# Kernel tuning notes

Hardware: AMD Instinct MI355X
Metric: run time of the kernel (lower is better)

## Reference

```python
import jax, jax.numpy as jnp
import numpy as np

E = 1024      # embedding_size
K = 64        # key_size
D = 64        # head_size
S = 1024      # context_size
V = 32000     # vocab_size
H = 16        # layer_size (heads per layer)
L = 8         # num_layers
B = 2


def _pe():
    pos = jnp.arange(S, dtype=jnp.float32)[:, None]
    i = jnp.arange(E, dtype=jnp.float32)[None, :]
    ang = pos / jnp.power(10000.0, 2.0 * i / E)
    return jnp.where((jnp.arange(E) % 2 == 0)[None, :], jnp.sin(ang), jnp.cos(ang))


def setup_inputs() -> dict:
    key = jax.random.key(0)
    ks = iter(jax.random.split(key, 32))
    s = 0.02
    n = lambda shape: jax.random.normal(next(ks), shape, dtype=jnp.float32) * s
    inp = {
        "tokens": jax.random.randint(next(ks), (B, S), 0, V),
        "emb": n((V, E)),
        "pe": _pe(),
        "k1w": n((L, H, K, E)), "k1b": n((L, H, K)),
        "k2w": n((L, H, K, K)), "k2b": n((L, H, K)),
        "q1w": n((L, H, K, E)), "q1b": n((L, H, K)),
        "q2w": n((L, H, K, K)), "q2b": n((L, H, K)),
        "vw": n((L, H, D, E)), "vb": n((L, H, D)),
        "lnw": jnp.ones((L, E), jnp.float32), "lnb": jnp.zeros((L, E), jnp.float32),
        "p1w": n((L, E, E)), "p1b": n((L, E)),
        "p2w": n((L, E, E)), "p2b": n((L, E)),
        "predw": n((V, E)), "predb": n((V,)),
    }
    return inp


def reference(tokens, emb, pe, k1w, k1b, k2w, k2b, q1w, q1b, q2w, q2b,
              vw, vb, lnw, lnb, p1w, p1b, p2w, p2b, predw, predb):
    relu = jax.nn.relu
    x = emb[tokens] + pe[:tokens.shape[1]]                       # [B,S,E]
    seq = tokens.shape[1]
    # Faithful to original: tril (past+diag) gets the -1e10 penalty.
    mask = jnp.tril(jnp.ones((seq, seq), x.dtype)) * -1e10
    for l in range(L):
        # two-layer ReLU MLPs for K and Q, batched over heads
        k = relu(jnp.einsum('bse,hke->bhsk', x, k1w[l]) + k1b[l][None, :, None, :])
        k = relu(jnp.einsum('bhsk,hjk->bhsj', k, k2w[l]) + k2b[l][None, :, None, :])
        q = relu(jnp.einsum('bse,hke->bhsk', x, q1w[l]) + q1b[l][None, :, None, :])
        q = relu(jnp.einsum('bhsk,hjk->bhsj', q, q2w[l]) + q2b[l][None, :, None, :])
        v = jnp.einsum('bse,hde->bhsd', x, vw[l]) + vb[l][None, :, None, :]
        scores = jnp.einsum('bhsk,bhtk->bhst', q, k) / (K ** 0.5) + mask
        w = jax.nn.softmax(scores, axis=-1)
        o = jnp.einsum('bhst,bhtd->bhsd', w, v)                  # [B,H,S,D]
        o = o.transpose(0, 2, 1, 3).reshape(x.shape[0], seq, H * D)
        y = x + o
        mu = y.mean(-1, keepdims=True)
        var = ((y - mu) ** 2).mean(-1, keepdims=True)
        yn = (y - mu) / jnp.sqrt(var + 1e-5) * lnw[l] + lnb[l]
        h1 = relu(yn @ p1w[l].T + p1b[l])
        x = relu(h1 @ p2w[l].T + p2b[l])
    logits = x @ predw.T + predb                                 # [B,S,V]
    return logits
```

## Files before the change

### kernel.cpp

```cpp
#include <hip/hip_runtime.h>


typedef __attribute__((ext_vector_type(8))) short bf16x8;
typedef __attribute__((ext_vector_type(4))) float f32x4;

#define L_ 8
#define S_ 1024
#define E_ 1024
#define B_ 2
#define H_ 16
#define V_ 32000
#define M_ 2048

__device__ __forceinline__ unsigned short f2b(float f) {
  union { float f; unsigned int u; } v; v.f = f;
  unsigned int r = v.u + 0x7FFFu + ((v.u >> 16) & 1u);
  return (unsigned short)(r >> 16);
}

#define GLDS16(gptr, lptr)                                                            \
  __builtin_amdgcn_global_load_lds(                                                   \
      (const __attribute__((address_space(1))) unsigned int*)(gptr),                  \
      (__attribute__((address_space(3))) unsigned int*)(lptr), 16, 0, 0)

__global__ void cvt_kernel(const float* __restrict__ src, unsigned short* __restrict__ dst) {
  size_t i = ((size_t)blockIdx.x * 256 + threadIdx.x) * 4;
  float4 v = *(const float4*)(src + i);
  unsigned short* d = dst + i;
  d[0] = f2b(v.x); d[1] = f2b(v.y); d[2] = f2b(v.z); d[3] = f2b(v.w);
}

__global__ void cvt_seg_kernel(const float* __restrict__ src, unsigned short* __restrict__ dst,
                               int perLayer, int dstStride, int dstOff) {
  size_t i = ((size_t)blockIdx.x * 256 + threadIdx.x) * 4;
  int l = (int)(i / perLayer);
  int off = (int)(i - (size_t)l * perLayer);
  float4 v = *(const float4*)(src + i);
  unsigned short* d = dst + (size_t)l * dstStride + dstOff + off;
  d[0] = f2b(v.x); d[1] = f2b(v.y); d[2] = f2b(v.z); d[3] = f2b(v.w);
}

__global__ void biascat_kernel(const float* __restrict__ k1b, const float* __restrict__ q1b,
                               const float* __restrict__ vb, float* __restrict__ bcat) {
  int i = blockIdx.x * 256 + threadIdx.x;
  int l = i / 3072, j = i - l * 3072;
  float v;
  if (j < 1024)      v = k1b[l * 1024 + j];
  else if (j < 2048) v = q1b[l * 1024 + j - 1024];
  else               v = vb [l * 1024 + j - 2048];
  bcat[i] = v;
}

__global__ void embed_kernel(const int* __restrict__ tokens, const float* __restrict__ emb,
                             const float* __restrict__ pe, float* __restrict__ x32,
                             unsigned short* __restrict__ xb) {
  int row = blockIdx.x;
  int s = row & (S_ - 1);
  int e0 = threadIdx.x * 4;
  int tok = tokens[row];
  float4 ev = *(const float4*)(emb + (size_t)tok * E_ + e0);
  float4 pv = *(const float4*)(pe + (size_t)s * E_ + e0);
  float4 v; v.x = ev.x + pv.x; v.y = ev.y + pv.y; v.z = ev.z + pv.z; v.w = ev.w + pv.w;
  *(float4*)(x32 + (size_t)row * E_ + e0) = v;
  ushort4 o; o.x = f2b(v.x); o.y = f2b(v.y); o.z = f2b(v.z); o.w = f2b(v.w);
  *(ushort4*)(xb + (size_t)row * E_ + e0) = o;
}

template <int BM, int RELU, int OBF, int OF32>
__global__ __launch_bounds__(256) void gemm97(
    const unsigned short* __restrict__ A, const unsigned short* __restrict__ W,
    const float* __restrict__ bias, unsigned short* __restrict__ Cb,
    float* __restrict__ Cf, int K, int N, int reluN) {
  constexpr int AR = BM / 64;
  constexpr int FM = (BM == 128) ? 4 : 2;
  constexpr int WMS = (BM == 128) ? 64 : 32;
  __shared__ __align__(16) unsigned short sA[BM * 32];
  __shared__ __align__(16) unsigned short sB[128 * 32];
  const int tid = threadIdx.x;
  const int lane = tid & 63, wave = tid >> 6;
  const int l16 = lane & 15, lhi = lane >> 4;

  const int gx = gridDim.x, nwg = gx * gridDim.y;
  int o = blockIdx.y * gx + blockIdx.x;
  int wg = ((nwg & 7) == 0) ? ((o & 7) * (nwg >> 3) + (o >> 3)) : o;
  const int row0 = (wg % gx) * BM, col0 = (wg / gx) * 128;

  const int wm = (wave >> 1) * WMS, wn = (wave & 1) * 64;

  const int srow = wave * 16 + (lane >> 2);
  const int scol = (lane & 3) * 8;

  f32x4 acc[FM][4] = {};

  for (int k0 = 0; k0 < K; k0 += 32) {
#pragma unroll
    for (int r = 0; r < AR; r++)
      GLDS16(A + (size_t)(row0 + r * 64 + srow) * K + k0 + scol,
             sA + r * 2048 + wave * 512);
#pragma unroll
    for (int r = 0; r < 2; r++)
      GLDS16(W + (size_t)(col0 + r * 64 + srow) * K + k0 + scol,
             sB + r * 2048 + wave * 512);
    __syncthreads();

    bf16x8 af[FM], bf[4];
#pragma unroll
    for (int i = 0; i < FM; i++)
      af[i] = *(const bf16x8*)(sA + (wm + i * 16 + l16) * 32 + lhi * 8);
#pragma unroll
    for (int j = 0; j < 4; j++)
      bf[j] = *(const bf16x8*)(sB + (wn + j * 16 + l16) * 32 + lhi * 8);
#pragma unroll
    for (int i = 0; i < FM; i++)
#pragma unroll
      for (int j = 0; j < 4; j++)
        acc[i][j] = __builtin_amdgcn_mfma_f32_16x16x32_bf16(bf[j], af[i], acc[i][j], 0, 0, 0);
    __syncthreads();
  }

#pragma unroll
  for (int j = 0; j < 4; j++) {
    const int colb = col0 + wn + j * 16 + lhi * 4;
    const float4 bv = *(const float4*)(bias + colb);
    const bool dorelu = (RELU == 1) || (RELU == 2 && colb < reluN);
#pragma unroll
    for (int i = 0; i < FM; i++) {
      const int row = row0 + wm + i * 16 + l16;
      float v0 = acc[i][j][0] + bv.x, v1 = acc[i][j][1] + bv.y;
      float v2 = acc[i][j][2] + bv.z, v3 = acc[i][j][3] + bv.w;
      if (dorelu) {
        v0 = fmaxf(v0, 0.f); v1 = fmaxf(v1, 0.f);
        v2 = fmaxf(v2, 0.f); v3 = fmaxf(v3, 0.f);
      }
      if (OBF) {
        ushort4 ob; ob.x = f2b(v0); ob.y = f2b(v1); ob.z = f2b(v2); ob.w = f2b(v3);
        *(ushort4*)(Cb + (size_t)row * N + colb) = ob;
      }
      if (OF32) {
        float4 of; of.x = v0; of.y = v1; of.z = v2; of.w = v3;
        *(float4*)(Cf + (size_t)row * N + colb) = of;
      }
    }
  }
}

__global__ __launch_bounds__(256) void k2q2_kernel(
    const unsigned short* __restrict__ kqv, const unsigned short* __restrict__ wk2,
    const unsigned short* __restrict__ wq2, const float* __restrict__ k2b,
    const float* __restrict__ q2b, unsigned short* __restrict__ kbuf,
    unsigned short* __restrict__ qbuf) {
  const int m0 = blockIdx.x * 64;
  const int h = blockIdx.y;
  const int which = blockIdx.z;
  const unsigned short* Ap = kqv + (which ? 1024 : 0) + h * 64;
  const unsigned short* Wp = (which ? wq2 : wk2) + h * 4096;
  const float* bias = (which ? q2b : k2b) + h * 64;
  unsigned short* out = (which ? qbuf : kbuf) + h * 64;
  const int lane = threadIdx.x & 63, wave = threadIdx.x >> 6;
  const int l16 = lane & 15, lhi = lane >> 4;
  const int mw = m0 + wave * 16;

  f32x4 acc[4] = {};
#pragma unroll
  for (int ks = 0; ks < 2; ks++) {
    bf16x8 a = *(const bf16x8*)(Ap + (size_t)(mw + l16) * 3072 + ks * 32 + (lhi << 3));
#pragma unroll
    for (int j = 0; j < 4; j++) {
      bf16x8 b = *(const bf16x8*)(Wp + (j * 16 + l16) * 64 + ks * 32 + (lhi << 3));
      acc[j] = __builtin_amdgcn_mfma_f32_16x16x32_bf16(a, b, acc[j], 0, 0, 0);
    }
  }
#pragma unroll
  for (int j = 0; j < 4; j++) {
    float bv = bias[j * 16 + l16];
#pragma unroll
    for (int r = 0; r < 4; r++) {
      int row = mw + (lhi << 2) + r;
      float v = fmaxf(acc[j][r] + bv, 0.f);
      out[(size_t)row * 1024 + j * 16 + l16] = f2b(v);
    }
  }
}

__global__ __launch_bounds__(256) void attn_kernel(
    const unsigned short* __restrict__ qbuf,
    const unsigned short* __restrict__ kbuf,
    const unsigned short* __restrict__ kqv,
    float* __restrict__ o32) {
  constexpr int LD = 72;
  __shared__ __align__(16) unsigned short sK[64 * LD];
  __shared__ __align__(16) unsigned short sV[64 * LD];
  __shared__ __align__(16) unsigned short sP[4 * 16 * LD];
  const int bx = blockIdx.x, h = blockIdx.y, b = blockIdx.z;
  const int tid = threadIdx.x, lane = tid & 63, wave = tid >> 6;
  const int l16 = lane & 15, lhi = lane >> 4;
  const int base = b * S_;

  const int qrow = bx * 64 + wave * 16 + l16;
  bf16x8 aq[2];
#pragma unroll
  for (int ks = 0; ks < 2; ks++)
    aq[ks] = *(const bf16x8*)(qbuf + (size_t)(base + qrow) * 1024 + h * 64 + ks * 32 + (lhi << 3));

  f32x4 oacc[4] = {};
  float mrun[4], lrun[4];
#pragma unroll
  for (int r = 0; r < 4; r++) { mrun[r] = -1e10f; lrun[r] = 0.f; }
  const int srow_base = bx * 64 + wave * 16 + (lhi << 2);

  for (int t0 = 0; t0 < S_; t0 += 64) {
    uint4 rk[2], rv[2];
#pragma unroll
    for (int r = 0; r < 2; r++) {
      int c = r * 256 + tid;
      int trow = c >> 3, c8 = (c & 7) << 3;
      rk[r] = *(const uint4*)(kbuf + (size_t)(base + t0 + trow) * 1024 + h * 64 + c8);
      rv[r] = *(const uint4*)(kqv + (size_t)(base + t0 + trow) * 3072 + 2048 + h * 64 + c8);
    }
    __syncthreads();
#pragma unroll
    for (int r = 0; r < 2; r++) {
      int c = r * 256 + tid;
      int trow = c >> 3, c8 = (c & 7) << 3;
      *(uint4*)(sK + trow * LD + c8) = rk[r];
      const unsigned short* ts = (const unsigned short*)&rv[r];
#pragma unroll
      for (int j = 0; j < 8; j++) sV[(c8 + j) * LD + trow] = ts[j];
    }
    __syncthreads();

    f32x4 sacc[4] = {};
#pragma unroll
    for (int ks = 0; ks < 2; ks++) {
#pragma unroll
      for (int nt = 0; nt < 4; nt++) {
        bf16x8 bk = *(const bf16x8*)(sK + (nt * 16 + l16) * LD + ks * 32 + (lhi << 3));
        sacc[nt] = __builtin_amdgcn_mfma_f32_16x16x32_bf16(aq[ks], bk, sacc[nt], 0, 0, 0);
      }
    }
    float p[4][4];
#pragma unroll
    for (int nt = 0; nt < 4; nt++) {
      int tcol = t0 + nt * 16 + l16;
#pragma unroll
      for (int r = 0; r < 4; r++) {
        float v = sacc[nt][r] * 0.125f;
        if (tcol <= srow_base + r) v = -1e10f;
        p[nt][r] = v;
      }
    }
#pragma unroll
    for (int r = 0; r < 4; r++) {
      float m = fmaxf(fmaxf(p[0][r], p[1][r]), fmaxf(p[2][r], p[3][r]));
#pragma unroll
      for (int off = 1; off < 16; off <<= 1) m = fmaxf(m, __shfl_xor(m, off, 16));
      float mnew = fmaxf(mrun[r], m);
      float alpha = __expf(mrun[r] - mnew);
      mrun[r] = mnew;
      float rs = 0.f;
#pragma unroll
      for (int nt = 0; nt < 4; nt++) {
        float e = __expf(p[nt][r] - mnew);
        p[nt][r] = e; rs += e;
      }
#pragma unroll
      for (int off = 1; off < 16; off <<= 1) rs += __shfl_xor(rs, off, 16);
      lrun[r] = lrun[r] * alpha + rs;
      oacc[0][r] *= alpha; oacc[1][r] *= alpha; oacc[2][r] *= alpha; oacc[3][r] *= alpha;
    }
    unsigned short* sPw = sP + wave * 16 * LD;
#pragma unroll
    for (int nt = 0; nt < 4; nt++)
#pragma unroll
      for (int r = 0; r < 4; r++)
        sPw[((lhi << 2) + r) * LD + nt * 16 + l16] = f2b(p[nt][r]);
#pragma unroll
    for (int ks = 0; ks < 2; ks++) {
      bf16x8 ap = *(const bf16x8*)(sPw + l16 * LD + ks * 32 + (lhi << 3));
#pragma unroll
      for (int nt = 0; nt < 4; nt++) {
        bf16x8 bv = *(const bf16x8*)(sV + (nt * 16 + l16) * LD + ks * 32 + (lhi << 3));
        oacc[nt] = __builtin_amdgcn_mfma_f32_16x16x32_bf16(ap, bv, oacc[nt], 0, 0, 0);
      }
    }
  }
#pragma unroll
  for (int nt = 0; nt < 4; nt++) {
#pragma unroll
    for (int r = 0; r < 4; r++) {
      int row = srow_base + r;
      o32[(size_t)(base + row) * 1024 + h * 64 + nt * 16 + l16] = oacc[nt][r] / lrun[r];
    }
  }
}

__global__ __launch_bounds__(256) void ln_kernel(
    const float* __restrict__ x32, const float* __restrict__ o32,
    const float* __restrict__ lnw, const float* __restrict__ lnb,
    unsigned short* __restrict__ yn) {
  __shared__ float red[8];
  const int row = blockIdx.x, tid = threadIdx.x;
  const int lane = tid & 63, wave = tid >> 6;
  const int e0 = tid * 4;
  float4 xv = *(const float4*)(x32 + (size_t)row * E_ + e0);
  float4 ov = *(const float4*)(o32 + (size_t)row * E_ + e0);
  float y0 = xv.x + ov.x, y1 = xv.y + ov.y, y2 = xv.z + ov.z, y3 = xv.w + ov.w;
  float s = y0 + y1 + y2 + y3;
  float sq = y0 * y0 + y1 * y1 + y2 * y2 + y3 * y3;
#pragma unroll
  for (int off = 32; off > 0; off >>= 1) {
    s += __shfl_xor(s, off, 64);
    sq += __shfl_xor(sq, off, 64);
  }
  if (lane == 0) { red[wave * 2] = s; red[wave * 2 + 1] = sq; }
  __syncthreads();
  float ts = red[0] + red[2] + red[4] + red[6];
  float tsq = red[1] + red[3] + red[5] + red[7];
  float mu = ts * (1.f / E_);
  float var = tsq * (1.f / E_) - mu * mu;
  float rstd = rsqrtf(var + 1e-5f);
  float4 gv = *(const float4*)(lnw + e0);
  float4 bv = *(const float4*)(lnb + e0);
  ushort4 o;
  o.x = f2b((y0 - mu) * rstd * gv.x + bv.x);
  o.y = f2b((y1 - mu) * rstd * gv.y + bv.y);
  o.z = f2b((y2 - mu) * rstd * gv.z + bv.z);
  o.w = f2b((y3 - mu) * rstd * gv.w + bv.w);
  *(ushort4*)(yn + (size_t)row * E_ + e0) = o;
}

extern "C" void kernel_launch(void* const* d_in, const int* in_sizes, int n_in,
                              void* d_out, int out_size, void* d_ws, size_t ws_size,
                              hipStream_t stream) {
  const int* tokens  = (const int*)d_in[0];
  const float* emb   = (const float*)d_in[1];
  const float* pe    = (const float*)d_in[2];
  const float* k1w   = (const float*)d_in[3];
  const float* k1b   = (const float*)d_in[4];
  const float* k2w   = (const float*)d_in[5];
  const float* k2b   = (const float*)d_in[6];
  const float* q1w   = (const float*)d_in[7];
  const float* q1b   = (const float*)d_in[8];
  const float* q2w   = (const float*)d_in[9];
  const float* q2b   = (const float*)d_in[10];
  const float* vw    = (const float*)d_in[11];
  const float* vb    = (const float*)d_in[12];
  const float* lnw   = (const float*)d_in[13];
  const float* lnb   = (const float*)d_in[14];
  const float* p1w   = (const float*)d_in[15];
  const float* p1b   = (const float*)d_in[16];
  const float* p2w   = (const float*)d_in[17];
  const float* p2b   = (const float*)d_in[18];
  const float* predw = (const float*)d_in[19];
  const float* predb = (const float*)d_in[20];
  float* out = (float*)d_out;

  char* p = (char*)d_ws;
  auto alloc = [&](size_t bytes) -> char* {
    char* r = p; p += (bytes + 255) & ~(size_t)255; return r;
  };
  unsigned short* wcat  = (unsigned short*)alloc((size_t)L_ * 3072 * 1024 * 2);
  unsigned short* wk2   = (unsigned short*)alloc((size_t)L_ * H_ * 64 * 64 * 2);
  unsigned short* wq2   = (unsigned short*)alloc((size_t)L_ * H_ * 64 * 64 * 2);
  unsigned short* wp1   = (unsigned short*)alloc((size_t)L_ * 1024 * 1024 * 2);
  unsigned short* wp2   = (unsigned short*)alloc((size_t)L_ * 1024 * 1024 * 2);
  unsigned short* wpred = (unsigned short*)alloc((size_t)V_ * 1024 * 2);
  float*          bcat  = (float*)alloc((size_t)L_ * 3072 * 4);
  float*          x32   = (float*)alloc((size_t)M_ * 1024 * 4);
  unsigned short* xb    = (unsigned short*)alloc((size_t)M_ * 1024 * 2);
  unsigned short* kqv   = (unsigned short*)alloc((size_t)M_ * 3072 * 2);
  unsigned short* kbuf  = (unsigned short*)alloc((size_t)M_ * 1024 * 2);
  unsigned short* qbuf  = (unsigned short*)alloc((size_t)M_ * 1024 * 2);
  float*          o32   = (float*)alloc((size_t)M_ * 1024 * 4);
  unsigned short* yn    = (unsigned short*)alloc((size_t)M_ * 1024 * 2);
  unsigned short* h1    = (unsigned short*)alloc((size_t)M_ * 1024 * 2);
  if ((size_t)(p - (char*)d_ws) > ws_size) return;

  cvt_seg_kernel<<<8192, 256, 0, stream>>>(k1w, wcat, 1048576, 3145728, 0);
  cvt_seg_kernel<<<8192, 256, 0, stream>>>(q1w, wcat, 1048576, 3145728, 1048576);
  cvt_seg_kernel<<<8192, 256, 0, stream>>>(vw,  wcat, 1048576, 3145728, 2097152);
  cvt_kernel<<<512, 256, 0, stream>>>(k2w, wk2);
  cvt_kernel<<<512, 256, 0, stream>>>(q2w, wq2);
  cvt_kernel<<<8192, 256, 0, stream>>>(p1w, wp1);
  cvt_kernel<<<8192, 256, 0, stream>>>(p2w, wp2);
  cvt_kernel<<<32000, 256, 0, stream>>>(predw, wpred);
  biascat_kernel<<<96, 256, 0, stream>>>(k1b, q1b, vb, bcat);

  embed_kernel<<<M_, 256, 0, stream>>>(tokens, emb, pe, x32, xb);

  for (int l = 0; l < L_; l++) {
    const unsigned short* wcat_l = wcat + (size_t)l * 3072 * 1024;
    const float* bcat_l = bcat + (size_t)l * 3072;
    const unsigned short* wk2_l = wk2 + (size_t)l * H_ * 64 * 64;
    const unsigned short* wq2_l = wq2 + (size_t)l * H_ * 64 * 64;
    const unsigned short* wp1_l = wp1 + (size_t)l * 1024 * 1024;
    const unsigned short* wp2_l = wp2 + (size_t)l * 1024 * 1024;

    gemm97<128, 2, 1, 0><<<dim3(16, 24), 256, 0, stream>>>(
        xb, wcat_l, bcat_l, kqv, nullptr, 1024, 3072, 2048);
    k2q2_kernel<<<dim3(32, 16, 2), 256, 0, stream>>>(
        kqv, wk2_l, wq2_l, k2b + l * 1024, q2b + l * 1024, kbuf, qbuf);
    attn_kernel<<<dim3(16, 16, 2), 256, 0, stream>>>(qbuf, kbuf, kqv, o32);
    ln_kernel<<<M_, 256, 0, stream>>>(x32, o32, lnw + l * 1024, lnb + l * 1024, yn);
    gemm97<64, 1, 1, 0><<<dim3(32, 8), 256, 0, stream>>>(
        yn, wp1_l, p1b + l * 1024, h1, nullptr, 1024, 1024, 0);
    gemm97<64, 1, 1, 1><<<dim3(32, 8), 256, 0, stream>>>(
        h1, wp2_l, p2b + l * 1024, xb, x32, 1024, 1024, 0);
  }

  gemm97<128, 0, 0, 1><<<dim3(16, 250), 256, 0, stream>>>(
      xb, wpred, predb, nullptr, out, 1024, V_, 0);
}
```

Measured before the change: 1.554 ms.

## Write transposed V from QKV GEMM and restructure attention to read global directly

The QKV GEMM epilogue now also writes V transposed per (batch, head) into a new buffer. The attention kernel drops its shared-memory staging of K and V and reads K and V^T fragments straight from global memory. It runs 128-thread blocks over 32-row query tiles, with a start offset that skips KV tiles the mask fully covers. The projection GEMMs switch to 64x64 tiles so more workgroups launch; the cost is scattered 2-byte stores for V^T and more global-load traffic in attention.

```diff
diff --git a/kernel.cpp b/kernel.cpp
--- a/kernel.cpp
+++ b/kernel.cpp
@@ -66,16 +66,18 @@
   *(ushort4*)(xb + (size_t)row * E_ + e0) = o;
 }
 
-template <int BM, int RELU, int OBF, int OF32>
+template <int BM, int BN, int RELU, int OBF, int OF32, int VT>
 __global__ __launch_bounds__(256) void gemm97(
     const unsigned short* __restrict__ A, const unsigned short* __restrict__ W,
     const float* __restrict__ bias, unsigned short* __restrict__ Cb,
-    float* __restrict__ Cf, int K, int N, int reluN) {
+    float* __restrict__ Cf, unsigned short* __restrict__ vTp,
+    int K, int N, int reluN) {
   constexpr int AR = BM / 64;
-  constexpr int FM = (BM == 128) ? 4 : 2;
-  constexpr int WMS = (BM == 128) ? 64 : 32;
+  constexpr int BR = BN / 64;
+  constexpr int FM = BM / 32;
+  constexpr int FN = BN / 32;
   __shared__ __align__(16) unsigned short sA[BM * 32];
-  __shared__ __align__(16) unsigned short sB[128 * 32];
+  __shared__ __align__(16) unsigned short sB[BN * 32];
   const int tid = threadIdx.x;
   const int lane = tid & 63, wave = tid >> 6;
   const int l16 = lane & 15, lhi = lane >> 4;
@@ -83,14 +85,14 @@
   const int gx = gridDim.x, nwg = gx * gridDim.y;
   int o = blockIdx.y * gx + blockIdx.x;
   int wg = ((nwg & 7) == 0) ? ((o & 7) * (nwg >> 3) + (o >> 3)) : o;
-  const int row0 = (wg % gx) * BM, col0 = (wg / gx) * 128;
-
-  const int wm = (wave >> 1) * WMS, wn = (wave & 1) * 64;
+  const int row0 = (wg % gx) * BM, col0 = (wg / gx) * BN;
+
+  const int wm = (wave >> 1) * (BM / 2), wn = (wave & 1) * (BN / 2);
 
   const int srow = wave * 16 + (lane >> 2);
   const int scol = (lane & 3) * 8;
 
-  f32x4 acc[FM][4] = {};
+  f32x4 acc[FM][FN] = {};
 
   for (int k0 = 0; k0 < K; k0 += 32) {
 #pragma unroll
@@ -98,28 +100,28 @@
       GLDS16(A + (size_t)(row0 + r * 64 + srow) * K + k0 + scol,
              sA + r * 2048 + wave * 512);
 #pragma unroll
-    for (int r = 0; r < 2; r++)
+    for (int r = 0; r < BR; r++)
       GLDS16(W + (size_t)(col0 + r * 64 + srow) * K + k0 + scol,
              sB + r * 2048 + wave * 512);
     __syncthreads();
 
-    bf16x8 af[FM], bf[4];
+    bf16x8 af[FM], bf[FN];
 #pragma unroll
     for (int i = 0; i < FM; i++)
       af[i] = *(const bf16x8*)(sA + (wm + i * 16 + l16) * 32 + lhi * 8);
 #pragma unroll
-    for (int j = 0; j < 4; j++)
+    for (int j = 0; j < FN; j++)
       bf[j] = *(const bf16x8*)(sB + (wn + j * 16 + l16) * 32 + lhi * 8);
 #pragma unroll
     for (int i = 0; i < FM; i++)
 #pragma unroll
-      for (int j = 0; j < 4; j++)
+      for (int j = 0; j < FN; j++)
         acc[i][j] = __builtin_amdgcn_mfma_f32_16x16x32_bf16(bf[j], af[i], acc[i][j], 0, 0, 0);
     __syncthreads();
   }
 
 #pragma unroll
-  for (int j = 0; j < 4; j++) {
+  for (int j = 0; j < FN; j++) {
     const int colb = col0 + wn + j * 16 + lhi * 4;
     const float4 bv = *(const float4*)(bias + colb);
     const bool dorelu = (RELU == 1) || (RELU == 2 && colb < reluN);
@@ -139,6 +141,14 @@
       if (OF32) {
         float4 of; of.x = v0; of.y = v1; of.z = v2; of.w = v3;
         *(float4*)(Cf + (size_t)row * N + colb) = of;
+      }
+      if (VT) {
+        if (colb - lhi * 4 >= 2048) {
+          const int hd0 = colb - 2048;
+          const int bq = row >> 10, s = row & 1023;
+          unsigned short* vr = vTp + ((size_t)(bq << 10) + hd0) * 1024 + s;
+          vr[0] = f2b(v0); vr[1024] = f2b(v1); vr[2048] = f2b(v2); vr[3072] = f2b(v3);
+        }
       }
     }
   }
@@ -182,21 +192,21 @@
   }
 }
 
-__global__ __launch_bounds__(256) void attn_kernel(
+__global__ __launch_bounds__(128) void attn_kernel(
     const unsigned short* __restrict__ qbuf,
     const unsigned short* __restrict__ kbuf,
-    const unsigned short* __restrict__ kqv,
+    const unsigned short* __restrict__ vT,
     float* __restrict__ o32) {
   constexpr int LD = 72;
-  __shared__ __align__(16) unsigned short sK[64 * LD];
-  __shared__ __align__(16) unsigned short sV[64 * LD];
-  __shared__ __align__(16) unsigned short sP[4 * 16 * LD];
-  const int bx = blockIdx.x, h = blockIdx.y, b = blockIdx.z;
-  const int tid = threadIdx.x, lane = tid & 63, wave = tid >> 6;
+  __shared__ __align__(16) unsigned short sP[2 * 16 * LD];
+  const int bid = blockIdx.x;
+  const int bh = bid & 31, qt = bid >> 5;
+  const int b = bh >> 4, h = bh & 15;
+  const int tid = threadIdx.x, lane = tid & 63, w = tid >> 6;
   const int l16 = lane & 15, lhi = lane >> 4;
   const int base = b * S_;
-
-  const int qrow = bx * 64 + wave * 16 + l16;
+  const int qrow = qt * 32 + w * 16 + l16;
+
   bf16x8 aq[2];
 #pragma unroll
   for (int ks = 0; ks < 2; ks++)
@@ -206,35 +216,19 @@
   float mrun[4], lrun[4];
 #pragma unroll
   for (int r = 0; r < 4; r++) { mrun[r] = -1e10f; lrun[r] = 0.f; }
-  const int srow_base = bx * 64 + wave * 16 + (lhi << 2);
-
-  for (int t0 = 0; t0 < S_; t0 += 64) {
-    uint4 rk[2], rv[2];
-#pragma unroll
-    for (int r = 0; r < 2; r++) {
-      int c = r * 256 + tid;
-      int trow = c >> 3, c8 = (c & 7) << 3;
-      rk[r] = *(const uint4*)(kbuf + (size_t)(base + t0 + trow) * 1024 + h * 64 + c8);
-      rv[r] = *(const uint4*)(kqv + (size_t)(base + t0 + trow) * 3072 + 2048 + h * 64 + c8);
-    }
-    __syncthreads();
-#pragma unroll
-    for (int r = 0; r < 2; r++) {
-      int c = r * 256 + tid;
-      int trow = c >> 3, c8 = (c & 7) << 3;
-      *(uint4*)(sK + trow * LD + c8) = rk[r];
-      const unsigned short* ts = (const unsigned short*)&rv[r];
-#pragma unroll
-      for (int j = 0; j < 8; j++) sV[(c8 + j) * LD + trow] = ts[j];
-    }
-    __syncthreads();
-
+  const int srow = qt * 32 + w * 16 + (lhi << 2);
+  const int t0s = (qt == 31) ? 0 : ((qt >> 1) << 6);
+
+  unsigned short* sPw = sP + w * 16 * LD;
+
+  for (int t0 = t0s; t0 < S_; t0 += 64) {
     f32x4 sacc[4] = {};
 #pragma unroll
     for (int ks = 0; ks < 2; ks++) {
 #pragma unroll
       for (int nt = 0; nt < 4; nt++) {
-        bf16x8 bk = *(const bf16x8*)(sK + (nt * 16 + l16) * LD + ks * 32 + (lhi << 3));
+        bf16x8 bk = *(const bf16x8*)(kbuf + (size_t)(base + t0 + nt * 16 + l16) * 1024 +
+                                     h * 64 + ks * 32 + (lhi << 3));
         sacc[nt] = __builtin_amdgcn_mfma_f32_16x16x32_bf16(aq[ks], bk, sacc[nt], 0, 0, 0);
       }
     }
@@ -245,7 +239,7 @@
 #pragma unroll
       for (int r = 0; r < 4; r++) {
         float v = sacc[nt][r] * 0.125f;
-        if (tcol <= srow_base + r) v = -1e10f;
+        if (tcol <= srow + r) v = -1e10f;
         p[nt][r] = v;
       }
     }
@@ -268,7 +262,6 @@
       lrun[r] = lrun[r] * alpha + rs;
       oacc[0][r] *= alpha; oacc[1][r] *= alpha; oacc[2][r] *= alpha; oacc[3][r] *= alpha;
     }
-    unsigned short* sPw = sP + wave * 16 * LD;
 #pragma unroll
     for (int nt = 0; nt < 4; nt++)
 #pragma unroll
@@ -279,7 +272,8 @@
       bf16x8 ap = *(const bf16x8*)(sPw + l16 * LD + ks * 32 + (lhi << 3));
 #pragma unroll
       for (int nt = 0; nt < 4; nt++) {
-        bf16x8 bv = *(const bf16x8*)(sV + (nt * 16 + l16) * LD + ks * 32 + (lhi << 3));
+        bf16x8 bv = *(const bf16x8*)(vT + (size_t)(bh * 64 + nt * 16 + l16) * 1024 +
+                                     t0 + ks * 32 + (lhi << 3));
         oacc[nt] = __builtin_amdgcn_mfma_f32_16x16x32_bf16(ap, bv, oacc[nt], 0, 0, 0);
       }
     }
@@ -288,7 +282,7 @@
   for (int nt = 0; nt < 4; nt++) {
 #pragma unroll
     for (int r = 0; r < 4; r++) {
-      int row = srow_base + r;
+      int row = srow + r;
       o32[(size_t)(base + row) * 1024 + h * 64 + nt * 16 + l16] = oacc[nt][r] / lrun[r];
     }
   }
@@ -371,6 +365,7 @@
   unsigned short* kqv   = (unsigned short*)alloc((size_t)M_ * 3072 * 2);
   unsigned short* kbuf  = (unsigned short*)alloc((size_t)M_ * 1024 * 2);
   unsigned short* qbuf  = (unsigned short*)alloc((size_t)M_ * 1024 * 2);
+  unsigned short* vTb   = (unsigned short*)alloc((size_t)32 * 64 * 1024 * 2);
   float*          o32   = (float*)alloc((size_t)M_ * 1024 * 4);
   unsigned short* yn    = (unsigned short*)alloc((size_t)M_ * 1024 * 2);
   unsigned short* h1    = (unsigned short*)alloc((size_t)M_ * 1024 * 2);
@@ -396,18 +391,18 @@
     const unsigned short* wp1_l = wp1 + (size_t)l * 1024 * 1024;
     const unsigned short* wp2_l = wp2 + (size_t)l * 1024 * 1024;
 
-    gemm97<128, 2, 1, 0><<<dim3(16, 24), 256, 0, stream>>>(
-        xb, wcat_l, bcat_l, kqv, nullptr, 1024, 3072, 2048);
+    gemm97<128, 128, 2, 1, 0, 1><<<dim3(16, 24), 256, 0, stream>>>(
+        xb, wcat_l, bcat_l, kqv, nullptr, vTb, 1024, 3072, 2048);
     k2q2_kernel<<<dim3(32, 16, 2), 256, 0, stream>>>(
         kqv, wk2_l, wq2_l, k2b + l * 1024, q2b + l * 1024, kbuf, qbuf);
-    attn_kernel<<<dim3(16, 16, 2), 256, 0, stream>>>(qbuf, kbuf, kqv, o32);
+    attn_kernel<<<1024, 128, 0, stream>>>(qbuf, kbuf, vTb, o32);
     ln_kernel<<<M_, 256, 0, stream>>>(x32, o32, lnw + l * 1024, lnb + l * 1024, yn);
-    gemm97<64, 1, 1, 0><<<dim3(32, 8), 256, 0, stream>>>(
-        yn, wp1_l, p1b + l * 1024, h1, nullptr, 1024, 1024, 0);
-    gemm97<64, 1, 1, 1><<<dim3(32, 8), 256, 0, stream>>>(
-        h1, wp2_l, p2b + l * 1024, xb, x32, 1024, 1024, 0);
-  }
-
-  gemm97<128, 0, 0, 1><<<dim3(16, 250), 256, 0, stream>>>(
-      xb, wpred, predb, nullptr, out, 1024, V_, 0);
-}
+    gemm97<64, 64, 1, 1, 0, 0><<<dim3(32, 16), 256, 0, stream>>>(
+        yn, wp1_l, p1b + l * 1024, h1, nullptr, nullptr, 1024, 1024, 0);
+    gemm97<64, 64, 1, 1, 1, 0><<<dim3(32, 16), 256, 0, stream>>>(
+        h1, wp2_l, p2b + l * 1024, xb, x32, nullptr, 1024, 1024, 0);
+  }
+
+  gemm97<128, 128, 0, 0, 1, 0><<<dim3(16, 250), 256, 0, stream>>>(
+      xb, wpred, predb, nullptr, out, nullptr, 1024, V_, 0);
+}
```

New measurement: 1.496 ms. 1.04x faster.
